# Kernel tuning notes

Measured on AMD Instinct MI355X. Metric: run time of the kernel, lower is better.

## Reference

```python
import jax, jax.numpy as jnp
import numpy as np

N_NODES = 100000
N_EDGES = 3200000
N_GRAPHS = 64


def setup_inputs() -> dict:
    key = jax.random.key(0)
    ks = jax.random.split(key, 9)
    x = jax.random.normal(ks[0], (N_NODES, 3), dtype=jnp.float32)
    edge_index = jax.random.randint(ks[1], (2, N_EDGES), 0, N_NODES, dtype=jnp.int64)
    batch = jnp.sort(jax.random.randint(ks[2], (N_NODES,), 0, N_GRAPHS, dtype=jnp.int64))
    s1 = 1.0 / np.sqrt(3.0)
    s2 = 1.0 / np.sqrt(64.0)
    W1 = jax.random.normal(ks[3], (3, 64), dtype=jnp.float32) * s1
    b1 = jax.random.normal(ks[4], (64,), dtype=jnp.float32) * 0.02
    W2 = jax.random.normal(ks[5], (64, 64), dtype=jnp.float32) * s2
    b2 = jax.random.normal(ks[6], (64,), dtype=jnp.float32) * 0.02
    Wr = jax.random.normal(ks[7], (64, 1), dtype=jnp.float32) * s2
    br = jax.random.normal(ks[8], (1,), dtype=jnp.float32) * 0.02
    return {"x": x, "edge_index": edge_index, "batch": batch,
            "W1": W1, "b1": b1, "W2": W2, "b2": b2, "Wr": Wr, "br": br}


def reference(x, edge_index, batch, W1, b1, W2, b2, Wr, br):
    N = x.shape[0]
    # GCN normalization with self-loops: A_hat = D^-1/2 (A+I) D^-1/2
    loop = jnp.arange(N, dtype=edge_index.dtype)
    src = jnp.concatenate([edge_index[0], loop])  # message sources
    dst = jnp.concatenate([edge_index[1], loop])  # aggregation targets
    deg = jax.ops.segment_sum(jnp.ones(src.shape, jnp.float32), dst, num_segments=N)
    dinv = jnp.where(deg > 0, jax.lax.rsqrt(deg), 0.0)
    norm = dinv[src] * dinv[dst]  # [E+N]

    def conv(h):  # h: [N, F] -> gather, scale, scatter-add
        return jax.ops.segment_sum(norm[:, None] * h[src], dst, num_segments=N)

    h = jax.nn.relu(conv(x @ W1) + b1)
    # dropout(p=0.5) is identity in eval mode
    h = jax.nn.relu(conv(h @ W2) + b2)
    # global mean pool over graphs
    counts = jax.ops.segment_sum(jnp.ones((N,), jnp.float32), batch, num_segments=N_GRAPHS)
    pooled = jax.ops.segment_sum(h, batch, num_segments=N_GRAPHS) / jnp.maximum(counts, 1.0)[:, None]
    return pooled @ Wr + br
```

## Files before the change

kernel.cpp:

```cpp
#include <hip/hip_runtime.h>

#define N_NODES  100000
#define N_EDGES  3200000
#define N_GRAPHS 64
#define NBUCK 391
#define BSH   8
#define TILE  4096
#define CSR_CAP 9216

typedef float v2f __attribute__((ext_vector_type(2)));

__device__ __forceinline__ unsigned pk8(float a, float b, float c, float d) {
    int r = 0;
    r = __builtin_amdgcn_cvt_pk_fp8_f32(a, b, r, false);
    r = __builtin_amdgcn_cvt_pk_fp8_f32(c, d, r, true);
    return (unsigned)r;
}
__device__ __forceinline__ void addfp8(float4& a, unsigned u) {
    v2f lo = __builtin_amdgcn_cvt_pk_f32_fp8((int)u, false);
    v2f hi = __builtin_amdgcn_cvt_pk_f32_fp8((int)u, true);
    a.x += lo[0]; a.y += lo[1]; a.z += hi[0]; a.w += hi[1];
}
__device__ __forceinline__ void fma4(float4& c, float s, const float4& w) {
    c.x += s * w.x; c.y += s * w.y; c.z += s * w.z; c.w += s * w.w;
}

__global__ __launch_bounds__(1024) void k_split(
        const int* __restrict__ src, const int* __restrict__ dst,
        int* __restrict__ gcur, unsigned int* __restrict__ ebuf, int E) {
    __shared__ int hist[512];
    __shared__ int excl_s[512];
    __shared__ int base[NBUCK];
    __shared__ int curs[NBUCK];
    __shared__ int wtot[8];
    __shared__ unsigned int stg[TILE];
    __shared__ unsigned short bkt[TILE];
    int t = threadIdx.x;
    if (t < 512) hist[t] = 0;
    __syncthreads();

    int e0 = blockIdx.x * TILE;
    int nvalid = min(TILE, E - e0);
    int es[4], ed[4];
#pragma unroll
    for (int k = 0; k < 4; ++k) {
        int i = e0 + t + k * 1024;
        if (i < E) {
            es[k] = src[i]; ed[k] = dst[i];
            atomicAdd(&hist[ed[k] >> BSH], 1);
        } else { es[k] = 0; ed[k] = -1; }
    }
    __syncthreads();
    int v = (t < 512) ? hist[t] : 0;
    int lane = t & 63, wvi = t >> 6;
    int val = v;
    for (int off = 1; off < 64; off <<= 1) {
        int u = __shfl_up(val, off);
        if (lane >= off) val += u;
    }
    if (t < 512 && lane == 63) wtot[wvi] = val;
    __syncthreads();
    if (t < 512) {
        int woff = 0;
        for (int w = 0; w < wvi; ++w) woff += wtot[w];
        int texcl = woff + val - v;
        excl_s[t] = texcl;
        if (t < NBUCK) {
            if (v > 0) base[t] = atomicAdd(&gcur[t], v);
            curs[t] = 0;
        }
    }
    __syncthreads();
#pragma unroll
    for (int k = 0; k < 4; ++k) {
        if (ed[k] >= 0) {
            int b = ed[k] >> BSH;
            int r = atomicAdd(&curs[b], 1);
            int pos = excl_s[b] + r;
            stg[pos] = ((unsigned)(ed[k] & 255) << 24) | (unsigned)es[k];
            bkt[pos] = (unsigned short)b;
        }
    }
    __syncthreads();
    for (int j = t; j < nvalid; j += 1024) {
        unsigned p = stg[j];
        int b = bkt[j];
        int pos = base[b] + (j - excl_s[b]);
        if (pos < CSR_CAP) ebuf[(size_t)b * CSR_CAP + pos] = p;
    }
}

__global__ __launch_bounds__(1024) void k_csr(
        const unsigned int* __restrict__ ebuf, const int* __restrict__ gcur,
        int* __restrict__ rowptr, float* __restrict__ dinv, float4* __restrict__ y4,
        const float* __restrict__ x, int* __restrict__ csr_src, int N) {
    __shared__ int ncnt[256];
    __shared__ int nbase[256];
    __shared__ int ncur[256];
    __shared__ int wtot[4];
    __shared__ int sbase;
    __shared__ int stg[CSR_CAP];
    int b = blockIdx.x, t = threadIdx.x;
    int node0 = b << BSH;
    int nodes = min(256, N - node0);
    int cntE = min(gcur[b], CSR_CAP);
    const unsigned int* eb = ebuf + (size_t)b * CSR_CAP;
    if (t < 64) {
        int acc = 0;
        for (int i = t; i < b; i += 64) acc += min(gcur[i], CSR_CAP);
        for (int off = 32; off > 0; off >>= 1) acc += __shfl_down(acc, off);
        if (t == 0) sbase = acc;
    }
    if (t < 256) { ncnt[t] = 0; ncur[t] = 0; }
    __syncthreads();
    int base = sbase;
    if (b == NBUCK - 1 && t == 0) rowptr[N_NODES] = base + cntE;
    for (int j = t; j < cntE; j += 1024) atomicAdd(&ncnt[(int)(eb[j] >> 24)], 1);
    __syncthreads();
    int v = (t < 256) ? ncnt[t] : 0;
    if (t < 256) {
        int lane = t & 63, wv = t >> 6;
        int val = v;
        for (int off = 1; off < 64; off <<= 1) {
            int u = __shfl_up(val, off);
            if (lane >= off) val += u;
        }
        if (lane == 63) wtot[wv] = val;
        __syncthreads();
        int woff = 0;
        for (int w = 0; w < wv; ++w) woff += wtot[w];
        int excl = woff + val - v;
        nbase[t] = excl;
        if (t < nodes) {
            int nn = node0 + t;
            rowptr[nn] = base + excl;
            float dn = rsqrtf((float)(v + 1));
            dinv[nn] = dn;
            y4[nn] = make_float4(dn * x[nn * 3 + 0], dn * x[nn * 3 + 1], dn * x[nn * 3 + 2], 0.f);
        }
    } else {
        __syncthreads();
    }
    __syncthreads();
    for (int j = t; j < cntE; j += 1024) {
        unsigned p = eb[j];
        int ln = (int)(p >> 24);
        int r = atomicAdd(&ncur[ln], 1);
        stg[nbase[ln] + r] = (int)(p & 0xFFFFFFu);
    }
    __syncthreads();
    for (int j = t; j < cntE; j += 1024) csr_src[(size_t)base + j] = stg[j];
}

__global__ __launch_bounds__(256) void k_agg3h1(
        const float4* __restrict__ y4, const int* __restrict__ csr_src,
        const int* __restrict__ rowptr, const float* __restrict__ dinv,
        const float* __restrict__ W1, const float* __restrict__ b1,
        uint4* __restrict__ Hs, int N) {
    int tid = blockIdx.x * blockDim.x + threadIdx.x;
    int n = tid >> 2, q = tid & 3;
    if (n >= N) return;
    int beg = rowptr[n], end = rowptr[n + 1];
    float4 a0 = make_float4(0.f, 0.f, 0.f, 0.f);
    float4 a1 = make_float4(0.f, 0.f, 0.f, 0.f);
    float4 a2 = make_float4(0.f, 0.f, 0.f, 0.f);
    float4 a3 = make_float4(0.f, 0.f, 0.f, 0.f);
    int c = beg + q;
    for (; c + 12 < end; c += 16) {
        int s0 = csr_src[c], s1 = csr_src[c + 4], s2 = csr_src[c + 8], s3 = csr_src[c + 12];
        float4 v0 = y4[s0], v1 = y4[s1], v2 = y4[s2], v3 = y4[s3];
        a0.x += v0.x; a0.y += v0.y; a0.z += v0.z;
        a1.x += v1.x; a1.y += v1.y; a1.z += v1.z;
        a2.x += v2.x; a2.y += v2.y; a2.z += v2.z;
        a3.x += v3.x; a3.y += v3.y; a3.z += v3.z;
    }
    for (; c < end; c += 4) {
        float4 v = y4[csr_src[c]];
        a0.x += v.x; a0.y += v.y; a0.z += v.z;
    }
    float rx = (a0.x + a1.x) + (a2.x + a3.x);
    float ry = (a0.y + a1.y) + (a2.y + a3.y);
    float rz = (a0.z + a1.z) + (a2.z + a3.z);
    for (int off = 1; off < 4; off <<= 1) {
        rx += __shfl_xor(rx, off);
        ry += __shfl_xor(ry, off);
        rz += __shfl_xor(rz, off);
    }
    float dn = dinv[n];
    float4 self = y4[n];
    float A0 = dn * (rx + self.x), A1 = dn * (ry + self.y), A2 = dn * (rz + self.z);
    unsigned vals[4];
#pragma unroll
    for (int g = 0; g < 4; ++g) {
        int f = 16 * q + 4 * g;
        float w0 = dn * fmaxf(A0 * W1[f]     + A1 * W1[64 + f]     + A2 * W1[128 + f]     + b1[f],     0.f);
        float w1 = dn * fmaxf(A0 * W1[f + 1] + A1 * W1[64 + f + 1] + A2 * W1[128 + f + 1] + b1[f + 1], 0.f);
        float w2 = dn * fmaxf(A0 * W1[f + 2] + A1 * W1[64 + f + 2] + A2 * W1[128 + f + 2] + b1[f + 2], 0.f);
        float w3 = dn * fmaxf(A0 * W1[f + 3] + A1 * W1[64 + f + 3] + A2 * W1[128 + f + 3] + b1[f + 3], 0.f);
        vals[g] = pk8(w0, w1, w2, w3);
    }
    Hs[(size_t)n * 4 + q] = make_uint4(vals[0], vals[1], vals[2], vals[3]);
}

__global__ __launch_bounds__(256) void k_agg(
        const unsigned int* __restrict__ Hs, const int* __restrict__ csr_src,
        const int* __restrict__ rowptr, const float* __restrict__ dinv,
        float* __restrict__ out, int N) {
    int tid = blockIdx.x * blockDim.x + threadIdx.x;
    int n = tid >> 4, q = tid & 15;
    if (n >= N) return;
    int lane = threadIdx.x & 63;
    int base = lane & ~15;
    int beg = rowptr[n], end = rowptr[n + 1];
    float4 acc0 = make_float4(0.f, 0.f, 0.f, 0.f);
    float4 acc1 = make_float4(0.f, 0.f, 0.f, 0.f);
    float4 acc2 = make_float4(0.f, 0.f, 0.f, 0.f);
    float4 acc3 = make_float4(0.f, 0.f, 0.f, 0.f);
    for (int c = beg; c < end; c += 16) {
        int myidx = csr_src[min(c + q, end - 1)];
        int m = min(16, end - c);
        int j = 0;
        for (; j + 4 <= m; j += 4) {
            int s0 = __shfl(myidx, base + j + 0);
            int s1 = __shfl(myidx, base + j + 1);
            int s2 = __shfl(myidx, base + j + 2);
            int s3 = __shfl(myidx, base + j + 3);
            unsigned u0 = Hs[(size_t)s0 * 16 + q];
            unsigned u1 = Hs[(size_t)s1 * 16 + q];
            unsigned u2 = Hs[(size_t)s2 * 16 + q];
            unsigned u3 = Hs[(size_t)s3 * 16 + q];
            addfp8(acc0, u0); addfp8(acc1, u1); addfp8(acc2, u2); addfp8(acc3, u3);
        }
        for (; j < m; ++j) {
            int s = __shfl(myidx, base + j);
            addfp8(acc0, Hs[(size_t)s * 16 + q]);
        }
    }
    addfp8(acc0, Hs[(size_t)n * 16 + q]);
    float dn = dinv[n];
    float4 r;
    r.x = dn * ((acc0.x + acc1.x) + (acc2.x + acc3.x));
    r.y = dn * ((acc0.y + acc1.y) + (acc2.y + acc3.y));
    r.z = dn * ((acc0.z + acc1.z) + (acc2.z + acc3.z));
    r.w = dn * ((acc0.w + acc1.w) + (acc2.w + acc3.w));
    ((float4*)(out + (size_t)n * 64))[q] = r;
}

__global__ __launch_bounds__(256) void k_mmpool(
        const float4* __restrict__ A4, const float4* __restrict__ W2v,
        const float* __restrict__ b2, const float* __restrict__ Wr,
        const int* __restrict__ batch, float* __restrict__ gsum,
        float* __restrict__ gcnt, int N) {
    __shared__ float4 W2s[1024];
    __shared__ float lsum[N_GRAPHS];
    __shared__ float lcnt[N_GRAPHS];
    int t = threadIdx.x;
    for (int i = t; i < 1024; i += 256) W2s[i] = W2v[i];
    if (t < N_GRAPHS) { lsum[t] = 0.f; lcnt[t] = 0.f; }
    __syncthreads();

    int f4 = t & 15;
    int ng = t >> 4;
    float4 bb = ((const float4*)b2)[f4];
    float4 wr = ((const float4*)Wr)[f4];
    int base = blockIdx.x * 128;

    for (int tile = 0; tile < 2; ++tile) {
        int n0 = base + tile * 64 + ng * 4;
        int m0 = min(n0 + 0, N - 1), m1 = min(n0 + 1, N - 1);
        int m2 = min(n0 + 2, N - 1), m3 = min(n0 + 3, N - 1);
        const float4* r0 = A4 + (size_t)m0 * 16;
        const float4* r1 = A4 + (size_t)m1 * 16;
        const float4* r2 = A4 + (size_t)m2 * 16;
        const float4* r3 = A4 + (size_t)m3 * 16;
        float4 c0 = make_float4(0.f, 0.f, 0.f, 0.f);
        float4 c1 = make_float4(0.f, 0.f, 0.f, 0.f);
        float4 c2 = make_float4(0.f, 0.f, 0.f, 0.f);
        float4 c3 = make_float4(0.f, 0.f, 0.f, 0.f);
#pragma unroll 4
        for (int ks = 0; ks < 16; ++ks) {
            float4 a0 = r0[ks], a1 = r1[ks], a2 = r2[ks], a3 = r3[ks];
            float4 w0 = W2s[(4 * ks + 0) * 16 + f4];
            float4 w1 = W2s[(4 * ks + 1) * 16 + f4];
            float4 w2 = W2s[(4 * ks + 2) * 16 + f4];
            float4 w3 = W2s[(4 * ks + 3) * 16 + f4];
            fma4(c0, a0.x, w0); fma4(c0, a0.y, w1); fma4(c0, a0.z, w2); fma4(c0, a0.w, w3);
            fma4(c1, a1.x, w0); fma4(c1, a1.y, w1); fma4(c1, a1.z, w2); fma4(c1, a1.w, w3);
            fma4(c2, a2.x, w0); fma4(c2, a2.y, w1); fma4(c2, a2.z, w2); fma4(c2, a2.w, w3);
            fma4(c3, a3.x, w0); fma4(c3, a3.y, w1); fma4(c3, a3.z, w2); fma4(c3, a3.w, w3);
        }
        float p0 = fmaxf(c0.x + bb.x, 0.f) * wr.x + fmaxf(c0.y + bb.y, 0.f) * wr.y +
                   fmaxf(c0.z + bb.z, 0.f) * wr.z + fmaxf(c0.w + bb.w, 0.f) * wr.w;
        float p1 = fmaxf(c1.x + bb.x, 0.f) * wr.x + fmaxf(c1.y + bb.y, 0.f) * wr.y +
                   fmaxf(c1.z + bb.z, 0.f) * wr.z + fmaxf(c1.w + bb.w, 0.f) * wr.w;
        float p2 = fmaxf(c2.x + bb.x, 0.f) * wr.x + fmaxf(c2.y + bb.y, 0.f) * wr.y +
                   fmaxf(c2.z + bb.z, 0.f) * wr.z + fmaxf(c2.w + bb.w, 0.f) * wr.w;
        float p3 = fmaxf(c3.x + bb.x, 0.f) * wr.x + fmaxf(c3.y + bb.y, 0.f) * wr.y +
                   fmaxf(c3.z + bb.z, 0.f) * wr.z + fmaxf(c3.w + bb.w, 0.f) * wr.w;
        for (int off = 8; off > 0; off >>= 1) {
            p0 += __shfl_down(p0, off);
            p1 += __shfl_down(p1, off);
            p2 += __shfl_down(p2, off);
            p3 += __shfl_down(p3, off);
        }
        if (f4 == 0) {
            if (n0 + 0 < N) { int g = batch[n0 + 0]; atomicAdd(&lsum[g], p0); atomicAdd(&lcnt[g], 1.f); }
            if (n0 + 1 < N) { int g = batch[n0 + 1]; atomicAdd(&lsum[g], p1); atomicAdd(&lcnt[g], 1.f); }
            if (n0 + 2 < N) { int g = batch[n0 + 2]; atomicAdd(&lsum[g], p2); atomicAdd(&lcnt[g], 1.f); }
            if (n0 + 3 < N) { int g = batch[n0 + 3]; atomicAdd(&lsum[g], p3); atomicAdd(&lcnt[g], 1.f); }
        }
    }
    __syncthreads();
    if (t < N_GRAPHS && lcnt[t] > 0.0f) {
        atomicAdd(&gsum[t], lsum[t]);
        atomicAdd(&gcnt[t], lcnt[t]);
    }
}

__global__ void k_out(const float* __restrict__ gsum, const float* __restrict__ gcnt,
                      const float* __restrict__ br, float* __restrict__ out) {
    int g = threadIdx.x;
    if (g < N_GRAPHS) out[g] = gsum[g] / fmaxf(gcnt[g], 1.0f) + br[0];
}

extern "C" void kernel_launch(void* const* d_in, const int* in_sizes, int n_in,
                              void* d_out, int out_size, void* d_ws, size_t ws_size,
                              hipStream_t stream) {
    const float* x     = (const float*)d_in[0];
    const int*   ei    = (const int*)d_in[1];
    const int*   batch = (const int*)d_in[2];
    const float* W1    = (const float*)d_in[3];
    const float* b1    = (const float*)d_in[4];
    const float* W2    = (const float*)d_in[5];
    const float* b2    = (const float*)d_in[6];
    const float* Wr    = (const float*)d_in[7];
    const float* br    = (const float*)d_in[8];
    float* out = (float*)d_out;

    const int N = N_NODES, E = N_EDGES;
    const int* src = ei;
    const int* dst = ei + E;

    char* w = (char*)d_ws;
    float* A        = (float*)w; w += (size_t)N * 64 * sizeof(float);
    unsigned int* Hs = (unsigned int*)w; w += (size_t)N * 64;
    int*   csr_src  = (int*)w;   w += (size_t)E * sizeof(int);
    float* dinv     = (float*)w; w += (size_t)N * sizeof(float);
    int*   rowptr   = (int*)w;   w += (size_t)(N + 1) * sizeof(int);
    int*   gcur     = (int*)w;   w += (size_t)NBUCK * sizeof(int);
    float* gsum     = (float*)w; w += N_GRAPHS * sizeof(float);
    float* gcnt     = (float*)w; w += N_GRAPHS * sizeof(float);
    float4* y4      = (float4*)w; w += (size_t)N * sizeof(float4);
    unsigned int* ebuf = (unsigned int*)A;

    hipMemsetAsync(gcur, 0, (size_t)NBUCK * sizeof(int), stream);
    hipMemsetAsync(gsum, 0, N_GRAPHS * sizeof(float), stream);
    hipMemsetAsync(gcnt, 0, N_GRAPHS * sizeof(float), stream);

    k_split<<<(E + TILE - 1) / TILE, 1024, 0, stream>>>(src, dst, gcur, ebuf, E);
    k_csr<<<NBUCK, 1024, 0, stream>>>(ebuf, gcur, rowptr, dinv, y4, x, csr_src, N);

    k_agg3h1<<<(N * 4 + 255) / 256, 256, 0, stream>>>(y4, csr_src, rowptr, dinv,
                                                      W1, b1, (uint4*)Hs, N);

    k_agg<<<(N * 16 + 255) / 256, 256, 0, stream>>>(Hs, csr_src, rowptr, dinv, A, N);
    k_mmpool<<<(N + 127) / 128, 256, 0, stream>>>((const float4*)A, (const float4*)W2,
                                                  b2, Wr, batch, gsum, gcnt, N);

    k_out<<<1, 64, 0, stream>>>(gsum, gcnt, br, out);
}
```

Before: 221.1 us.

## Split each CSR bucket across two blocks and merge the small memsets

The CSR-building kernel now launches two blocks per bucket, and each block scatters only the edges whose destination falls in its half of the bucket's 256 nodes. Both blocks still recount all edges to get prefix offsets. The three small memsets become one contiguous memset covering gcur, gsum and gcnt. This should raise parallelism in k_csr (391 blocks is few for the GPU) and cut launch overhead, but each block still reads the full bucket twice, so global reads double.

```diff
diff --git a/kernel.cpp b/kernel.cpp
--- a/kernel.cpp
+++ b/kernel.cpp
@@ -96,13 +96,17 @@
         const float* __restrict__ x, int* __restrict__ csr_src, int N) {
     __shared__ int ncnt[256];
     __shared__ int nbase[256];
-    __shared__ int ncur[256];
+    __shared__ int ncur[128];
     __shared__ int wtot[4];
     __shared__ int sbase;
     __shared__ int stg[CSR_CAP];
-    int b = blockIdx.x, t = threadIdx.x;
-    int node0 = b << BSH;
-    int nodes = min(256, N - node0);
+    int blk = blockIdx.x, t = threadIdx.x;
+    int b = blk >> 1;
+    int h = blk & 1;
+    int bnode0 = b << BSH;
+    int node0 = bnode0 + (h << 7);
+    int nodesAll = min(256, N - bnode0);
+    int nodes = max(0, min(128, nodesAll - (h << 7)));
     int cntE = min(gcur[b], CSR_CAP);
     const unsigned int* eb = ebuf + (size_t)b * CSR_CAP;
     if (t < 64) {
@@ -111,10 +115,11 @@
         for (int off = 32; off > 0; off >>= 1) acc += __shfl_down(acc, off);
         if (t == 0) sbase = acc;
     }
-    if (t < 256) { ncnt[t] = 0; ncur[t] = 0; }
+    if (t < 256) ncnt[t] = 0;
+    if (t < 128) ncur[t] = 0;
     __syncthreads();
     int base = sbase;
-    if (b == NBUCK - 1 && t == 0) rowptr[N_NODES] = base + cntE;
+    if (b == NBUCK - 1 && h == 1 && t == 0) rowptr[N_NODES] = base + cntE;
     for (int j = t; j < cntE; j += 1024) atomicAdd(&ncnt[(int)(eb[j] >> 24)], 1);
     __syncthreads();
     int v = (t < 256) ? ncnt[t] : 0;
@@ -131,8 +136,9 @@
         for (int w = 0; w < wv; ++w) woff += wtot[w];
         int excl = woff + val - v;
         nbase[t] = excl;
-        if (t < nodes) {
-            int nn = node0 + t;
+        int ln = t - (h << 7);
+        if (ln >= 0 && ln < nodes) {
+            int nn = node0 + ln;
             rowptr[nn] = base + excl;
             float dn = rsqrtf((float)(v + 1));
             dinv[nn] = dn;
@@ -142,14 +148,18 @@
         __syncthreads();
     }
     __syncthreads();
+    int start = h ? nbase[128] : 0;
+    int cntH = h ? (cntE - nbase[128]) : nbase[128];
     for (int j = t; j < cntE; j += 1024) {
         unsigned p = eb[j];
         int ln = (int)(p >> 24);
-        int r = atomicAdd(&ncur[ln], 1);
-        stg[nbase[ln] + r] = (int)(p & 0xFFFFFFu);
-    }
-    __syncthreads();
-    for (int j = t; j < cntE; j += 1024) csr_src[(size_t)base + j] = stg[j];
+        if ((ln >> 7) == h) {
+            int r = atomicAdd(&ncur[ln & 127], 1);
+            stg[nbase[ln] - start + r] = (int)(p & 0xFFFFFFu);
+        }
+    }
+    __syncthreads();
+    for (int j = t; j < cntH; j += 1024) csr_src[(size_t)(base + start) + j] = stg[j];
 }
 
 __global__ __launch_bounds__(256) void k_agg3h1(
@@ -353,12 +363,10 @@
     float4* y4      = (float4*)w; w += (size_t)N * sizeof(float4);
     unsigned int* ebuf = (unsigned int*)A;
 
-    hipMemsetAsync(gcur, 0, (size_t)NBUCK * sizeof(int), stream);
-    hipMemsetAsync(gsum, 0, N_GRAPHS * sizeof(float), stream);
-    hipMemsetAsync(gcnt, 0, N_GRAPHS * sizeof(float), stream);
+    hipMemsetAsync(gcur, 0, (size_t)(NBUCK + 2 * N_GRAPHS) * sizeof(int), stream);
 
     k_split<<<(E + TILE - 1) / TILE, 1024, 0, stream>>>(src, dst, gcur, ebuf, E);
-    k_csr<<<NBUCK, 1024, 0, stream>>>(ebuf, gcur, rowptr, dinv, y4, x, csr_src, N);
+    k_csr<<<2 * NBUCK, 1024, 0, stream>>>(ebuf, gcur, rowptr, dinv, y4, x, csr_src, N);
 
     k_agg3h1<<<(N * 4 + 255) / 256, 256, 0, stream>>>(y4, csr_src, rowptr, dinv,
                                                       W1, b1, (uint4*)Hs, N);
```

After: 221.9 us. About the same (+0.4%).
